# Performance work log

Hardware: AMD Instinct MI355X
Metric: run time of the kernel (lower is better)

The kernel has to match this reference:

```python
import jax, jax.numpy as jnp
import numpy as np


def setup_inputs() -> dict:
    key = jax.random.key(0)
    kq, kk, kv = jax.random.split(key, 3)
    b, n, h, d = 1, 8192, 8, 64
    return {
        "query": jax.random.normal(kq, (b, n, h, d), dtype=jnp.float32),
        "key": jax.random.normal(kk, (b, n, h, d), dtype=jnp.float32),
        "value": jax.random.normal(kv, (b, n, h, d), dtype=jnp.float32),
        "ring_size": 4,
    }


def _ring_attention(q, k, v, ring_size):
    # q,k,v: [b, n, h, d]. Emulates the ring: K/V split into ring_size chunks,
    # processed sequentially with online-softmax rescaling (non-causal).
    b, n, h, d = q.shape
    cs = n // ring_size  # chunk_size
    scale = 1.0 / jnp.sqrt(jnp.asarray(d, q.dtype))
    # [ring, b, cs, h, d]
    k_chunks = jnp.moveaxis(k.reshape(b, ring_size, cs, h, d), 1, 0)
    v_chunks = jnp.moveaxis(v.reshape(b, ring_size, cs, h, d), 1, 0)

    out0 = jnp.zeros((b, h, n, d), q.dtype)
    m0 = jnp.full((b, h, n, 1), -jnp.inf, q.dtype)
    s0 = jnp.zeros((b, h, n, 1), q.dtype)

    def step(carry, kv_chunk):
        out, m, s = carry
        kc, vc = kv_chunk  # [b, cs, h, d]
        scores = jnp.einsum("bqhd,bkhd->bhqk", q, kc) * scale  # [b,h,n,cs]
        chunk_max = scores.max(axis=-1, keepdims=True)
        new_max = jnp.maximum(m, chunk_max)
        corr = jnp.exp(m - new_max)  # 0 at first step since m=-inf
        exp_scores = jnp.exp(scores - new_max)
        out = out * corr + jnp.einsum("bhqk,bkhd->bhqd", exp_scores, vc)
        s = s * corr + exp_scores.sum(axis=-1, keepdims=True)
        return (out, new_max, s), None

    (out, _, s), _ = jax.lax.scan(step, (out0, m0, s0), (k_chunks, v_chunks))
    out = out / s
    return jnp.swapaxes(out, 1, 2)  # [b, n, h, d]


def reference(query, key, value, ring_size):
    return _ring_attention(query, key, value, ring_size)
```

## Files before the change

kernel.cpp:

```cpp
#include <hip/hip_runtime.h>
#include <hip/hip_bf16.h>

typedef __attribute__((ext_vector_type(8))) short bf16x8;
typedef __attribute__((ext_vector_type(8))) unsigned short u16x8;
typedef __attribute__((ext_vector_type(16))) float f32x16;
typedef __attribute__((ext_vector_type(4))) unsigned int u32x4;

#define MFMA32(a, b, c) __builtin_amdgcn_mfma_f32_32x32x16_bf16(a, b, c, 0, 0, 0)

constexpr int NSEQ = 8192;
constexpr int NH   = 8;
constexpr int DIM  = 64;
constexpr int KVB  = 64;
constexpr int QB   = 128;
constexpr int NT   = NSEQ / KVB;
constexpr int SLAB = KVB * DIM;
constexpr float SCL2 = 0.18033688011112042f;

__device__ __forceinline__ unsigned cvt_pk(float lo, float hi) {
    unsigned r;
    asm("v_cvt_pk_bf16_f32 %0, %1, %2" : "=v"(r) : "v"(lo), "v"(hi));
    return r;
}
__device__ __forceinline__ float exp2f_fast(float x) {
    float r;
    asm("v_exp_f32 %0, %1" : "=v"(r) : "v"(x));
    return r;
}
__device__ __forceinline__ void pl32swap(unsigned& a, unsigned& b) {
    asm("v_permlane32_swap_b32 %0, %1" : "+v"(a), "+v"(b));
}
__device__ __forceinline__ int swz(int row, int col) {
    return row * 64 + ((((col >> 3) ^ row) & 7) << 3) + (col & 7);
}

__global__ __launch_bounds__(256, 4)
void prep_kernel(const float* __restrict__ Kg, const float* __restrict__ Vg,
                 unsigned short* __restrict__ Kws, unsigned short* __restrict__ Vws) {
    __shared__ float Vf[64][65];
    const int tid = threadIdx.x;
    const int bid = blockIdx.x;
    if (bid < 1024) {
        const int h = bid >> 7, t = bid & 127;
        unsigned short* dst = Kws + (size_t)bid * SLAB;
#pragma unroll
        for (int j = 0; j < 2; ++j) {
            const int m = tid * 2 + j;
            const int r = m >> 3, s = m & 7, c = s ^ (r & 7);
            const float* src = Kg + ((size_t)(t * 64 + r) * NH + h) * DIM + c * 8;
            float4 a = ((const float4*)src)[0];
            float4 b = ((const float4*)src)[1];
            u32x4 w;
            w[0] = cvt_pk(a.x, a.y); w[1] = cvt_pk(a.z, a.w);
            w[2] = cvt_pk(b.x, b.y); w[3] = cvt_pk(b.z, b.w);
            *(u32x4*)(dst + m * 8) = w;
        }
    } else {
        const int hb = bid - 1024;
        const int h = hb >> 7, t = hb & 127;
        const int key = tid >> 2, dc = (tid & 3) * 16;
        const float* src = Vg + ((size_t)(t * 64 + key) * NH + h) * DIM + dc;
#pragma unroll
        for (int i = 0; i < 4; ++i) {
            float4 a = ((const float4*)src)[i];
            Vf[key][dc + i * 4 + 0] = a.x; Vf[key][dc + i * 4 + 1] = a.y;
            Vf[key][dc + i * 4 + 2] = a.z; Vf[key][dc + i * 4 + 3] = a.w;
        }
        __syncthreads();
        unsigned short* dst = Vws + (size_t)hb * SLAB;
#pragma unroll
        for (int j = 0; j < 2; ++j) {
            const int m = tid * 2 + j;
            const int d = m >> 3, s = m & 7, c = s ^ (d & 7);
            u32x4 w;
            w[0] = cvt_pk(Vf[c * 8 + 0][d], Vf[c * 8 + 1][d]);
            w[1] = cvt_pk(Vf[c * 8 + 2][d], Vf[c * 8 + 3][d]);
            w[2] = cvt_pk(Vf[c * 8 + 4][d], Vf[c * 8 + 5][d]);
            w[3] = cvt_pk(Vf[c * 8 + 6][d], Vf[c * 8 + 7][d]);
            *(u32x4*)(dst + m * 8) = w;
        }
    }
}

__global__ __launch_bounds__(256, 2)
void fa_kernel(const float* __restrict__ Qg, const unsigned short* __restrict__ Kws,
               const unsigned short* __restrict__ Vws, float* __restrict__ Og) {
    __shared__ unsigned short Kb[2][SLAB];
    __shared__ unsigned short Vb[2][SLAB];

    const int tid  = threadIdx.x;
    const int lane = tid & 63;
    const int wave = tid >> 6;
    const int la31 = lane & 31;
    const int hi   = lane >> 5;
    const int head  = blockIdx.x & 7;
    const int qtile = blockIdx.x >> 3;
    const int q     = qtile * QB + wave * 32 + la31;

    bf16x8 qf[4];
#pragma unroll
    for (int kd = 0; kd < 4; ++kd) {
        const float* qp = Qg + ((size_t)q * NH + head) * DIM + kd * 16 + hi * 8;
        float4 a = ((const float4*)qp)[0];
        float4 b = ((const float4*)qp)[1];
        u32x4 w;
        w[0] = cvt_pk(a.x * SCL2, a.y * SCL2);
        w[1] = cvt_pk(a.z * SCL2, a.w * SCL2);
        w[2] = cvt_pk(b.x * SCL2, b.y * SCL2);
        w[3] = cvt_pk(b.z * SCL2, b.w * SCL2);
        qf[kd] = __builtin_bit_cast(bf16x8, w);
    }

    const unsigned short* ksl = Kws + (size_t)head * NT * SLAB + tid * 16;
    const unsigned short* vsl = Vws + (size_t)head * NT * SLAB + tid * 16;

    f32x16 oacc[2];
#pragma unroll
    for (int nt = 0; nt < 2; ++nt)
#pragma unroll
        for (int i = 0; i < 16; ++i) oacc[nt][i] = 0.f;
    float m_run = -1e30f, l_run = 0.f;

    u16x8 kr0 = *(const u16x8*)ksl, kr1 = *(const u16x8*)(ksl + 8);
    u16x8 vr0 = *(const u16x8*)vsl, vr1 = *(const u16x8*)(vsl + 8);
    ksl += SLAB; vsl += SLAB;

    for (int t = 0; t < NT; ++t) {
        const int cur = t & 1;
        *(u16x8*)&Kb[cur][tid * 16]     = kr0;
        *(u16x8*)&Kb[cur][tid * 16 + 8] = kr1;
        *(u16x8*)&Vb[cur][tid * 16]     = vr0;
        *(u16x8*)&Vb[cur][tid * 16 + 8] = vr1;
        __syncthreads();
        if (t + 1 < NT) {
            kr0 = *(const u16x8*)ksl; kr1 = *(const u16x8*)(ksl + 8);
            vr0 = *(const u16x8*)vsl; vr1 = *(const u16x8*)(vsl + 8);
            ksl += SLAB; vsl += SLAB;
        }
        const unsigned short* Kbase = &Kb[cur][0];
        const unsigned short* Vbase = &Vb[cur][0];

        f32x16 s0, s1;
#pragma unroll
        for (int i = 0; i < 16; ++i) { s0[i] = 0.f; s1[i] = 0.f; }
        __builtin_amdgcn_s_setprio(1);
#pragma unroll
        for (int kd = 0; kd < 4; ++kd) {
            bf16x8 k0 = *(const bf16x8*)(Kbase + swz(la31, kd * 16 + hi * 8));
            bf16x8 k1 = *(const bf16x8*)(Kbase + swz(32 + la31, kd * 16 + hi * 8));
            s0 = MFMA32(k0, qf[kd], s0);
            s1 = MFMA32(k1, qf[kd], s1);
        }
        __builtin_amdgcn_s_setprio(0);

        float pmv[16];
#pragma unroll
        for (int i = 0; i < 16; ++i) pmv[i] = fmaxf(s0[i], s1[i]);
#pragma unroll
        for (int st = 8; st >= 1; st >>= 1)
#pragma unroll
            for (int i = 0; i < 8; ++i)
                if (i < st) pmv[i] = fmaxf(pmv[i], pmv[i + st]);
        float pm = pmv[0];
        pm = fmaxf(pm, __shfl_xor(pm, 32));

        if (__any(pm > m_run + 8.f)) {
            float mnew = fmaxf(m_run, pm);
            float corr = exp2f_fast(m_run - mnew);
            m_run = mnew;
            l_run *= corr;
#pragma unroll
            for (int i = 0; i < 16; ++i) { oacc[0][i] *= corr; oacc[1][i] *= corr; }
        }

#pragma unroll
        for (int kb = 0; kb < 2; ++kb) {
            const f32x16& s = kb ? s1 : s0;
            float p[16];
#pragma unroll
            for (int i = 0; i < 16; ++i) p[i] = exp2f_fast(s[i] - m_run);
            float ts[8];
#pragma unroll
            for (int i = 0; i < 8; ++i) ts[i] = p[i] + p[i + 8];
#pragma unroll
            for (int i = 0; i < 4; ++i) ts[i] += ts[i + 4];
            l_run += (ts[0] + ts[1]) + (ts[2] + ts[3]);
            unsigned A[8];
#pragma unroll
            for (int j = 0; j < 8; ++j) A[j] = cvt_pk(p[2 * j], p[2 * j + 1]);
            pl32swap(A[0], A[2]); pl32swap(A[1], A[3]);
            pl32swap(A[4], A[6]); pl32swap(A[5], A[7]);
            u32x4 f0v; f0v[0] = A[0]; f0v[1] = A[1]; f0v[2] = A[2]; f0v[3] = A[3];
            u32x4 f1v; f1v[0] = A[4]; f1v[1] = A[5]; f1v[2] = A[6]; f1v[3] = A[7];
            bf16x8 frag[2] = { __builtin_bit_cast(bf16x8, f0v), __builtin_bit_cast(bf16x8, f1v) };

            __builtin_amdgcn_s_setprio(1);
#pragma unroll
            for (int ksl2 = 0; ksl2 < 2; ++ksl2) {
                const int ksg = kb * 2 + ksl2;
                bf16x8 vf0 = *(const bf16x8*)(Vbase + swz(la31, ksg * 16 + hi * 8));
                bf16x8 vf1 = *(const bf16x8*)(Vbase + swz(32 + la31, ksg * 16 + hi * 8));
                oacc[0] = MFMA32(vf0, frag[ksl2], oacc[0]);
                oacc[1] = MFMA32(vf1, frag[ksl2], oacc[1]);
            }
            __builtin_amdgcn_s_setprio(0);
        }
    }

    {
        float l_tot = l_run + __shfl_xor(l_run, 32);
        float inv = __builtin_amdgcn_rcpf(l_tot);
        float* obase = Og + ((size_t)q * NH + head) * DIM;
#pragma unroll
        for (int nt = 0; nt < 2; ++nt)
#pragma unroll
            for (int rq = 0; rq < 4; ++rq) {
                float4 o;
                o.x = oacc[nt][rq * 4 + 0] * inv;
                o.y = oacc[nt][rq * 4 + 1] * inv;
                o.z = oacc[nt][rq * 4 + 2] * inv;
                o.w = oacc[nt][rq * 4 + 3] * inv;
                *(float4*)(obase + nt * 32 + rq * 8 + hi * 4) = o;
            }
    }
}

__global__ __launch_bounds__(256, 2)
void fb_kernel(const float* __restrict__ Qg, const float* __restrict__ Kg,
               const float* __restrict__ Vg, float* __restrict__ Og) {
    __shared__ unsigned short Kl[KVB][DIM];
    __shared__ unsigned short Vt[DIM][KVB];
    unsigned short* Kbase = &Kl[0][0];
    unsigned short* Vbase = &Vt[0][0];
    const int tid  = threadIdx.x;
    const int lane = tid & 63;
    const int wave = tid >> 6;
    const int la31 = lane & 31;
    const int hi   = lane >> 5;
    const int head  = blockIdx.x & 7;
    const int qtile = blockIdx.x >> 3;
    const int q     = qtile * QB + wave * 32 + la31;
    bf16x8 qf[4];
#pragma unroll
    for (int kd = 0; kd < 4; ++kd) {
        const float* qp = Qg + ((size_t)q * NH + head) * DIM + kd * 16 + hi * 8;
        float4 a = ((const float4*)qp)[0];
        float4 b = ((const float4*)qp)[1];
        u32x4 w;
        w[0] = cvt_pk(a.x * SCL2, a.y * SCL2);
        w[1] = cvt_pk(a.z * SCL2, a.w * SCL2);
        w[2] = cvt_pk(b.x * SCL2, b.y * SCL2);
        w[3] = cvt_pk(b.z * SCL2, b.w * SCL2);
        qf[kd] = __builtin_bit_cast(bf16x8, w);
    }
    const int ksrow = tid & 63;
    const int kscol = (tid >> 6) * 16;
    const int vpair = tid & 31;
    const int vcg   = tid >> 5;
    const float* kptr  = Kg + ((size_t)ksrow * NH + head) * DIM + kscol;
    const float* vptr0 = Vg + ((size_t)(2 * vpair) * NH + head) * DIM + vcg * 8;
    const float* vptr1 = vptr0 + NH * DIM;
    constexpr size_t STRIDE = (size_t)KVB * NH * DIM;
    const int kIdx0 = swz(ksrow, kscol);
    const int kIdx1 = swz(ksrow, kscol + 8);
    f32x16 oacc[2];
#pragma unroll
    for (int nt = 0; nt < 2; ++nt)
#pragma unroll
        for (int i = 0; i < 16; ++i) oacc[nt][i] = 0.f;
    float m_run = -1e30f, l_run = 0.f;
    float4 kr0 = ((const float4*)kptr)[0], kr1 = ((const float4*)kptr)[1];
    float4 kr2 = ((const float4*)kptr)[2], kr3 = ((const float4*)kptr)[3];
    float4 va0 = ((const float4*)vptr0)[0], va1 = ((const float4*)vptr0)[1];
    float4 vb0 = ((const float4*)vptr1)[0], vb1 = ((const float4*)vptr1)[1];
    kptr += STRIDE; vptr0 += STRIDE; vptr1 += STRIDE;
    for (int t = 0; t < NT; ++t) {
        __syncthreads();
        {
            u32x4 w;
            w[0] = cvt_pk(kr0.x, kr0.y); w[1] = cvt_pk(kr0.z, kr0.w);
            w[2] = cvt_pk(kr1.x, kr1.y); w[3] = cvt_pk(kr1.z, kr1.w);
            *(u32x4*)(Kbase + kIdx0) = w;
            w[0] = cvt_pk(kr2.x, kr2.y); w[1] = cvt_pk(kr2.z, kr2.w);
            w[2] = cvt_pk(kr3.x, kr3.y); w[3] = cvt_pk(kr3.z, kr3.w);
            *(u32x4*)(Kbase + kIdx1) = w;
        }
        {
            *(unsigned*)(Vbase + swz(vcg * 8 + 0, 2 * vpair)) = cvt_pk(va0.x, vb0.x);
            *(unsigned*)(Vbase + swz(vcg * 8 + 1, 2 * vpair)) = cvt_pk(va0.y, vb0.y);
            *(unsigned*)(Vbase + swz(vcg * 8 + 2, 2 * vpair)) = cvt_pk(va0.z, vb0.z);
            *(unsigned*)(Vbase + swz(vcg * 8 + 3, 2 * vpair)) = cvt_pk(va0.w, vb0.w);
            *(unsigned*)(Vbase + swz(vcg * 8 + 4, 2 * vpair)) = cvt_pk(va1.x, vb1.x);
            *(unsigned*)(Vbase + swz(vcg * 8 + 5, 2 * vpair)) = cvt_pk(va1.y, vb1.y);
            *(unsigned*)(Vbase + swz(vcg * 8 + 6, 2 * vpair)) = cvt_pk(va1.z, vb1.z);
            *(unsigned*)(Vbase + swz(vcg * 8 + 7, 2 * vpair)) = cvt_pk(va1.w, vb1.w);
        }
        __syncthreads();
        if (t + 1 < NT) {
            kr0 = ((const float4*)kptr)[0]; kr1 = ((const float4*)kptr)[1];
            kr2 = ((const float4*)kptr)[2]; kr3 = ((const float4*)kptr)[3];
            va0 = ((const float4*)vptr0)[0]; va1 = ((const float4*)vptr0)[1];
            vb0 = ((const float4*)vptr1)[0]; vb1 = ((const float4*)vptr1)[1];
            kptr += STRIDE; vptr0 += STRIDE; vptr1 += STRIDE;
        }
        f32x16 s0, s1;
#pragma unroll
        for (int i = 0; i < 16; ++i) { s0[i] = 0.f; s1[i] = 0.f; }
        __builtin_amdgcn_s_setprio(1);
#pragma unroll
        for (int kd = 0; kd < 4; ++kd) {
            bf16x8 k0 = *(const bf16x8*)(Kbase + swz(la31, kd * 16 + hi * 8));
            bf16x8 k1 = *(const bf16x8*)(Kbase + swz(32 + la31, kd * 16 + hi * 8));
            s0 = MFMA32(k0, qf[kd], s0);
            s1 = MFMA32(k1, qf[kd], s1);
        }
        __builtin_amdgcn_s_setprio(0);
        float pmv[16];
#pragma unroll
        for (int i = 0; i < 16; ++i) pmv[i] = fmaxf(s0[i], s1[i]);
#pragma unroll
        for (int st = 8; st >= 1; st >>= 1)
#pragma unroll
            for (int i = 0; i < 8; ++i)
                if (i < st) pmv[i] = fmaxf(pmv[i], pmv[i + st]);
        float pm = pmv[0];
        pm = fmaxf(pm, __shfl_xor(pm, 32));
        if (__any(pm > m_run + 8.f)) {
            float mnew = fmaxf(m_run, pm);
            float corr = exp2f_fast(m_run - mnew);
            m_run = mnew;
            l_run *= corr;
#pragma unroll
            for (int i = 0; i < 16; ++i) { oacc[0][i] *= corr; oacc[1][i] *= corr; }
        }
#pragma unroll
        for (int kb = 0; kb < 2; ++kb) {
            const f32x16& s = kb ? s1 : s0;
            float p[16];
#pragma unroll
            for (int i = 0; i < 16; ++i) p[i] = exp2f_fast(s[i] - m_run);
            float ts[8];
#pragma unroll
            for (int i = 0; i < 8; ++i) ts[i] = p[i] + p[i + 8];
#pragma unroll
            for (int i = 0; i < 4; ++i) ts[i] += ts[i + 4];
            l_run += (ts[0] + ts[1]) + (ts[2] + ts[3]);
            unsigned A[8];
#pragma unroll
            for (int j = 0; j < 8; ++j) A[j] = cvt_pk(p[2 * j], p[2 * j + 1]);
            pl32swap(A[0], A[2]); pl32swap(A[1], A[3]);
            pl32swap(A[4], A[6]); pl32swap(A[5], A[7]);
            u32x4 f0v; f0v[0] = A[0]; f0v[1] = A[1]; f0v[2] = A[2]; f0v[3] = A[3];
            u32x4 f1v; f1v[0] = A[4]; f1v[1] = A[5]; f1v[2] = A[6]; f1v[3] = A[7];
            bf16x8 frag[2] = { __builtin_bit_cast(bf16x8, f0v), __builtin_bit_cast(bf16x8, f1v) };
            __builtin_amdgcn_s_setprio(1);
#pragma unroll
            for (int ksl = 0; ksl < 2; ++ksl) {
                const int ksg = kb * 2 + ksl;
                bf16x8 vf0 = *(const bf16x8*)(Vbase + swz(la31, ksg * 16 + hi * 8));
                bf16x8 vf1 = *(const bf16x8*)(Vbase + swz(32 + la31, ksg * 16 + hi * 8));
                oacc[0] = MFMA32(vf0, frag[ksl], oacc[0]);
                oacc[1] = MFMA32(vf1, frag[ksl], oacc[1]);
            }
            __builtin_amdgcn_s_setprio(0);
        }
    }
    {
        float l_tot = l_run + __shfl_xor(l_run, 32);
        float inv = __builtin_amdgcn_rcpf(l_tot);
        float* obase = Og + ((size_t)q * NH + head) * DIM;
#pragma unroll
        for (int nt = 0; nt < 2; ++nt)
#pragma unroll
            for (int rq = 0; rq < 4; ++rq) {
                float4 o;
                o.x = oacc[nt][rq * 4 + 0] * inv;
                o.y = oacc[nt][rq * 4 + 1] * inv;
                o.z = oacc[nt][rq * 4 + 2] * inv;
                o.w = oacc[nt][rq * 4 + 3] * inv;
                *(float4*)(obase + nt * 32 + rq * 8 + hi * 4) = o;
            }
    }
}

extern "C" void kernel_launch(void* const* d_in, const int* in_sizes, int n_in,
                              void* d_out, int out_size, void* d_ws, size_t ws_size,
                              hipStream_t stream) {
    const float* q = (const float*)d_in[0];
    const float* k = (const float*)d_in[1];
    const float* v = (const float*)d_in[2];
    float* out = (float*)d_out;
    constexpr size_t KV_WS = 2ull * NH * NT * SLAB * sizeof(unsigned short);
    if (ws_size >= KV_WS) {
        unsigned short* Kws = (unsigned short*)d_ws;
        unsigned short* Vws = Kws + (size_t)NH * NT * SLAB;
        hipLaunchKernelGGL(prep_kernel, dim3(2048), dim3(256), 0, stream, k, v, Kws, Vws);
        hipLaunchKernelGGL(fa_kernel, dim3(512), dim3(256), 0, stream, q, Kws, Vws, out);
    } else {
        hipLaunchKernelGGL(fb_kernel, dim3(512), dim3(256), 0, stream, q, k, v, out);
    }
}
```

Baseline: 204.0 us.

## Split KV loop across two wave groups per block and merge partial softmax states

The attention block grows from 256 to 512 threads. Two groups of four waves each process half of the KV tiles for the same 128 queries, with separate double-buffered LDS slabs per group. At the end, the second group writes its partial output accumulators and running max and sum to LDS, and the first group merges them with online-softmax rescaling. The goal is to shorten the serial KV loop and raise the number of resident waves so latency is hidden better. The cost is twice the LDS per block, a merge epilogue, and a 512,4 launch bound that tightens the register budget and may cause spills.

```diff
diff --git a/kernel.cpp b/kernel.cpp
--- a/kernel.cpp
+++ b/kernel.cpp
@@ -14,6 +14,7 @@
 constexpr int KVB  = 64;
 constexpr int QB   = 128;
 constexpr int NT   = NSEQ / KVB;
+constexpr int NTH  = NT / 2;
 constexpr int SLAB = KVB * DIM;
 constexpr float SCL2 = 0.18033688011112042f;
 
@@ -82,20 +83,23 @@
     }
 }
 
-__global__ __launch_bounds__(256, 2)
+__global__ __launch_bounds__(512, 4)
 void fa_kernel(const float* __restrict__ Qg, const unsigned short* __restrict__ Kws,
                const unsigned short* __restrict__ Vws, float* __restrict__ Og) {
-    __shared__ unsigned short Kb[2][SLAB];
-    __shared__ unsigned short Vb[2][SLAB];
+    __shared__ unsigned short Kb[2][2][SLAB];
+    __shared__ unsigned short Vb[2][2][SLAB];
 
     const int tid  = threadIdx.x;
     const int lane = tid & 63;
     const int wave = tid >> 6;
+    const int half = wave >> 2;
+    const int qw   = wave & 3;
     const int la31 = lane & 31;
     const int hi   = lane >> 5;
+    const int halftid = tid & 255;
     const int head  = blockIdx.x & 7;
     const int qtile = blockIdx.x >> 3;
-    const int q     = qtile * QB + wave * 32 + la31;
+    const int q     = qtile * QB + qw * 32 + la31;
 
     bf16x8 qf[4];
 #pragma unroll
@@ -111,8 +115,8 @@
         qf[kd] = __builtin_bit_cast(bf16x8, w);
     }
 
-    const unsigned short* ksl = Kws + (size_t)head * NT * SLAB + tid * 16;
-    const unsigned short* vsl = Vws + (size_t)head * NT * SLAB + tid * 16;
+    const unsigned short* ksl = Kws + ((size_t)head * NT + (size_t)half * NTH) * SLAB + halftid * 8;
+    const unsigned short* vsl = Vws + ((size_t)head * NT + (size_t)half * NTH) * SLAB + halftid * 8;
 
     f32x16 oacc[2];
 #pragma unroll
@@ -121,24 +125,24 @@
         for (int i = 0; i < 16; ++i) oacc[nt][i] = 0.f;
     float m_run = -1e30f, l_run = 0.f;
 
-    u16x8 kr0 = *(const u16x8*)ksl, kr1 = *(const u16x8*)(ksl + 8);
-    u16x8 vr0 = *(const u16x8*)vsl, vr1 = *(const u16x8*)(vsl + 8);
+    u16x8 kr0 = *(const u16x8*)ksl, kr1 = *(const u16x8*)(ksl + 2048);
+    u16x8 vr0 = *(const u16x8*)vsl, vr1 = *(const u16x8*)(vsl + 2048);
     ksl += SLAB; vsl += SLAB;
 
-    for (int t = 0; t < NT; ++t) {
+    for (int t = 0; t < NTH; ++t) {
         const int cur = t & 1;
-        *(u16x8*)&Kb[cur][tid * 16]     = kr0;
-        *(u16x8*)&Kb[cur][tid * 16 + 8] = kr1;
-        *(u16x8*)&Vb[cur][tid * 16]     = vr0;
-        *(u16x8*)&Vb[cur][tid * 16 + 8] = vr1;
+        *(u16x8*)&Kb[half][cur][halftid * 8]        = kr0;
+        *(u16x8*)&Kb[half][cur][2048 + halftid * 8] = kr1;
+        *(u16x8*)&Vb[half][cur][halftid * 8]        = vr0;
+        *(u16x8*)&Vb[half][cur][2048 + halftid * 8] = vr1;
         __syncthreads();
-        if (t + 1 < NT) {
-            kr0 = *(const u16x8*)ksl; kr1 = *(const u16x8*)(ksl + 8);
-            vr0 = *(const u16x8*)vsl; vr1 = *(const u16x8*)(vsl + 8);
+        if (t + 1 < NTH) {
+            kr0 = *(const u16x8*)ksl; kr1 = *(const u16x8*)(ksl + 2048);
+            vr0 = *(const u16x8*)vsl; vr1 = *(const u16x8*)(vsl + 2048);
             ksl += SLAB; vsl += SLAB;
         }
-        const unsigned short* Kbase = &Kb[cur][0];
-        const unsigned short* Vbase = &Vb[cur][0];
+        const unsigned short* Kbase = &Kb[half][cur][0];
+        const unsigned short* Vbase = &Vb[half][cur][0];
 
         f32x16 s0, s1;
 #pragma unroll
@@ -207,9 +211,33 @@
         }
     }
 
-    {
-        float l_tot = l_run + __shfl_xor(l_run, 32);
-        float inv = __builtin_amdgcn_rcpf(l_tot);
+    __syncthreads();
+    float* mrgO  = (float*)&Kb[0][0][0];
+    float* mrgML = (float*)&Vb[0][0][0];
+    const int idx = qw * 64 + lane;
+    if (half) {
+#pragma unroll
+        for (int i = 0; i < 16; ++i) {
+            mrgO[i * 256 + idx]        = oacc[0][i];
+            mrgO[(16 + i) * 256 + idx] = oacc[1][i];
+        }
+        mrgML[idx]       = m_run;
+        mrgML[256 + idx] = l_run;
+    }
+    __syncthreads();
+    if (!half) {
+        const float m1 = mrgML[idx], l1 = mrgML[256 + idx];
+        const float mnew = fmaxf(m_run, m1);
+        const float c0 = exp2f_fast(m_run - mnew);
+        const float c1 = exp2f_fast(m1 - mnew);
+        float lt = l_run * c0 + l1 * c1;
+#pragma unroll
+        for (int i = 0; i < 16; ++i) {
+            oacc[0][i] = oacc[0][i] * c0 + mrgO[i * 256 + idx] * c1;
+            oacc[1][i] = oacc[1][i] * c0 + mrgO[(16 + i) * 256 + idx] * c1;
+        }
+        const float l_tot = lt + __shfl_xor(lt, 32);
+        const float inv = __builtin_amdgcn_rcpf(l_tot);
         float* obase = Og + ((size_t)q * NH + head) * DIM;
 #pragma unroll
         for (int nt = 0; nt < 2; ++nt)
@@ -395,7 +423,7 @@
         unsigned short* Kws = (unsigned short*)d_ws;
         unsigned short* Vws = Kws + (size_t)NH * NT * SLAB;
         hipLaunchKernelGGL(prep_kernel, dim3(2048), dim3(256), 0, stream, k, v, Kws, Vws);
-        hipLaunchKernelGGL(fa_kernel, dim3(512), dim3(256), 0, stream, q, Kws, Vws, out);
+        hipLaunchKernelGGL(fa_kernel, dim3(512), dim3(512), 0, stream, q, Kws, Vws, out);
     } else {
         hipLaunchKernelGGL(fb_kernel, dim3(512), dim3(256), 0, stream, q, k, v, out);
     }
```

Result: slower. 208.5 us (+2.2%).
